# Kernel optimization log

Hardware: AMD Instinct MI355X
Metric: run time of the kernel (lower is better)

## Reference

```python
import jax, jax.numpy as jnp
import numpy as np

DROPOUT_P = 0.1


def setup_inputs() -> dict:
    key = jax.random.key(0)
    kq, kk, kv, km = jax.random.split(key, 4)
    B, H, S, D = 8, 16, 1024, 64
    query = jax.random.normal(kq, (B, H, S, D), dtype=jnp.float32)
    key_t = jax.random.normal(kk, (B, H, S, D), dtype=jnp.float32)
    value = jax.random.normal(kv, (B, H, S, D), dtype=jnp.float32)
    mask = jax.random.randint(km, (B, 1, S, S), 0, 2, dtype=jnp.int32)
    return {"query": query, "key": key_t, "value": value, "mask": mask}


def reference(query, key, value, mask):
    d_k = query.shape[-1]
    # scores: [B, H, S, S]
    scores = jnp.einsum("bhqd,bhkd->bhqk", query, key) / jnp.sqrt(
        jnp.asarray(d_k, dtype=query.dtype)
    )
    scores = jnp.where(mask == 0, jnp.asarray(-jnp.inf, dtype=scores.dtype), scores)
    attn_weights = jax.nn.softmax(scores, axis=-1)
    # deterministic dropout (train-mode semantics, fixed RNG)
    drop_key = jax.random.fold_in(jax.random.key(42), 7)
    keep = jax.random.bernoulli(drop_key, 1.0 - DROPOUT_P, attn_weights.shape)
    attn_weights = jnp.where(keep, attn_weights / (1.0 - DROPOUT_P), 0.0)
    output = jnp.einsum("bhqk,bhkd->bhqd", attn_weights, value)
    return (output, attn_weights)
```

## Files before the change

kernel.cpp:

```cpp
#include <hip/hip_runtime.h>


constexpr int Bc = 8, Hc = 16, Sc = 1024, Dc = 64;
constexpr int TQ  = 8;
constexpr int WTP = 12;

typedef float v4f __attribute__((ext_vector_type(4)));

#define TF_ROUND(x0, x1, r) { x0 += x1; x1 = ((x1 << (r)) | (x1 >> (32 - (r)))); x1 ^= x0; }

__host__ __device__ __forceinline__ void threefry2x32(unsigned k0, unsigned k1,
                                                      unsigned x0, unsigned x1,
                                                      unsigned& o0, unsigned& o1) {
  const unsigned k2 = k0 ^ k1 ^ 0x1BD11BDAu;
  x0 += k0; x1 += k1;
  TF_ROUND(x0, x1, 13) TF_ROUND(x0, x1, 15) TF_ROUND(x0, x1, 26) TF_ROUND(x0, x1, 6)
  x0 += k1; x1 += k2 + 1u;
  TF_ROUND(x0, x1, 17) TF_ROUND(x0, x1, 29) TF_ROUND(x0, x1, 16) TF_ROUND(x0, x1, 24)
  x0 += k2; x1 += k0 + 2u;
  TF_ROUND(x0, x1, 13) TF_ROUND(x0, x1, 15) TF_ROUND(x0, x1, 26) TF_ROUND(x0, x1, 6)
  x0 += k0; x1 += k1 + 3u;
  TF_ROUND(x0, x1, 17) TF_ROUND(x0, x1, 29) TF_ROUND(x0, x1, 16) TF_ROUND(x0, x1, 24)
  x0 += k1; x1 += k2 + 4u;
  TF_ROUND(x0, x1, 13) TF_ROUND(x0, x1, 15) TF_ROUND(x0, x1, 26) TF_ROUND(x0, x1, 6)
  x0 += k2; x1 += k0 + 5u;
  o0 = x0; o1 = x1;
}

__global__ __launch_bounds__(256, 4)
void attn_fused(const float* __restrict__ Qg, const float* __restrict__ Kg,
                const float* __restrict__ Vg, const int* __restrict__ Mg,
                float* __restrict__ Og, float* __restrict__ Ag,
                unsigned key0, unsigned key1)
{
  __shared__ __align__(16) float WTh[512][WTP];
  __shared__ float REDm[4][8];
  __shared__ float REDs[4][8];

  const unsigned orig = blockIdx.x;
  const unsigned wg   = (orig & 7u) * 2048u + (orig >> 3);
  const int q0 = (int)(wg & 127u) * TQ;
  const int h  = (int)(wg >> 7) & 15;
  const int b  = (int)(wg >> 11);

  const int tid = threadIdx.x;
  const int w   = tid >> 6;
  const int l   = tid & 63;
  const int kl  = w * 64 + l;
  const size_t bh = (size_t)b * Hc + h;

  const float* __restrict__ Kb = Kg + bh * Sc * Dc;
  const float* __restrict__ Vb = Vg + bh * Sc * Dc;
  const float* __restrict__ Qb = Qg + bh * Sc * Dc + (size_t)q0 * Dc;

  unsigned mbits = 0u;
  {
    const int* __restrict__ mc = Mg + (size_t)b * Sc * Sc + (size_t)q0 * Sc + kl;
    #pragma unroll
    for (int kb = 0; kb < 4; ++kb)
      #pragma unroll
      for (int q = 0; q < 8; ++q)
        mbits |= (mc[(size_t)q * Sc + kb * 256] != 0) ? (1u << (kb * 8 + q)) : 0u;
  }

  unsigned keep = 0u;
  const unsigned ibase = ((unsigned)((b * Hc + h) * Sc + q0)) * (unsigned)Sc
                         + (unsigned)kl;
  #pragma unroll 8
  for (int t2 = 0; t2 < 32; ++t2) {
    const int kb = t2 >> 3, q = t2 & 7;
    unsigned o0, o1;
    threefry2x32(key0, key1, 0u, ibase + (unsigned)(q * Sc + kb * 256), o0, o1);
    const unsigned bits = o0 ^ o1;
    const float u = __uint_as_float((bits >> 9) | 0x3f800000u) - 1.0f;
    keep |= (u < 0.9f) ? (1u << t2) : 0u;
  }

  float sv[4][8];
  #pragma unroll
  for (int kb = 0; kb < 4; ++kb)
    #pragma unroll
    for (int q = 0; q < 8; ++q) sv[kb][q] = 0.f;

  #pragma unroll 1
  for (int ds = 0; ds < 16; ++ds) {
    float4 qv[8];
    #pragma unroll
    for (int q = 0; q < 8; ++q)
      qv[q] = *(const float4*)(Qb + (size_t)q * Dc + ds * 4);
    #pragma unroll
    for (int kb = 0; kb < 4; ++kb) {
      const float4 kv = *(const float4*)(Kb + (size_t)(kb * 256 + kl) * Dc + ds * 4);
      #pragma unroll
      for (int q = 0; q < 8; ++q) {
        sv[kb][q] = fmaf(kv.x, qv[q].x, sv[kb][q]);
        sv[kb][q] = fmaf(kv.y, qv[q].y, sv[kb][q]);
        sv[kb][q] = fmaf(kv.z, qv[q].z, sv[kb][q]);
        sv[kb][q] = fmaf(kv.w, qv[q].w, sv[kb][q]);
      }
    }
  }

  const float NEG = -__builtin_inff();
  #pragma unroll
  for (int kb = 0; kb < 4; ++kb)
    #pragma unroll
    for (int q = 0; q < 8; ++q) {
      const float s = sv[kb][q] * 0.125f;
      sv[kb][q] = ((mbits >> (kb * 8 + q)) & 1u) ? s : NEG;
    }

  float mx[8];
  #pragma unroll
  for (int q = 0; q < 8; ++q) {
    float m = fmaxf(fmaxf(sv[0][q], sv[1][q]), fmaxf(sv[2][q], sv[3][q]));
    #pragma unroll
    for (int off = 32; off > 0; off >>= 1) m = fmaxf(m, __shfl_xor(m, off));
    if (l == 0) REDm[w][q] = m;
  }
  __syncthreads();
  #pragma unroll
  for (int q = 0; q < 8; ++q)
    mx[q] = fmaxf(fmaxf(REDm[0][q], REDm[1][q]), fmaxf(REDm[2][q], REDm[3][q]));

  #pragma unroll
  for (int kb = 0; kb < 4; ++kb)
    #pragma unroll
    for (int q = 0; q < 8; ++q)
      sv[kb][q] = __expf(sv[kb][q] - mx[q]);
  #pragma unroll
  for (int q = 0; q < 8; ++q) {
    float s = (sv[0][q] + sv[1][q]) + (sv[2][q] + sv[3][q]);
    #pragma unroll
    for (int off = 32; off > 0; off >>= 1) s += __shfl_xor(s, off);
    if (l == 0) REDs[w][q] = s;
  }
  __syncthreads();
  float inv9[8];
  #pragma unroll
  for (int q = 0; q < 8; ++q)
    inv9[q] = 1.0f / (((REDs[0][q] + REDs[1][q]) + (REDs[2][q] + REDs[3][q])) * 0.9f);

  float* __restrict__ Arow = Ag + bh * (size_t)Sc * Sc + (size_t)q0 * Sc + kl;
  #pragma unroll
  for (int kb = 0; kb < 4; ++kb)
    #pragma unroll
    for (int q = 0; q < 8; ++q) {
      const float wv = ((keep >> (kb * 8 + q)) & 1u) ? sv[kb][q] * inv9[q] : 0.f;
      sv[kb][q] = wv;
      __builtin_nontemporal_store(wv, &Arow[(size_t)q * Sc + kb * 256]);
    }

  const int ks = tid & 15;
  const int dq = tid >> 4;
  float4 acc[8];
  #pragma unroll
  for (int q = 0; q < 8; ++q) acc[q] = make_float4(0.f, 0.f, 0.f, 0.f);

#define ACCQ(qi, wq) { acc[qi].x = fmaf(wq, vv.x, acc[qi].x); \
                       acc[qi].y = fmaf(wq, vv.y, acc[qi].y); \
                       acc[qi].z = fmaf(wq, vv.z, acc[qi].z); \
                       acc[qi].w = fmaf(wq, vv.w, acc[qi].w); }
#define PV_COMPUTE(halfc)                                                    \
    _Pragma("unroll 4")                                                      \
    for (int i = 0; i < 32; ++i) {                                           \
      const int kr = i * 16 + ks;                                            \
      const float4 vv = *(const float4*)(Vb + (size_t)((halfc) * 512 + kr) * Dc + dq * 4); \
      const float4 lo = *(const float4*)&WTh[kr][0];                         \
      const float4 hi = *(const float4*)&WTh[kr][4];                         \
      ACCQ(0, lo.x) ACCQ(1, lo.y) ACCQ(2, lo.z) ACCQ(3, lo.w)                \
      ACCQ(4, hi.x) ACCQ(5, hi.y) ACCQ(6, hi.z) ACCQ(7, hi.w)                \
    }

  *(float4*)&WTh[kl][0]       = make_float4(sv[0][0], sv[0][1], sv[0][2], sv[0][3]);
  *(float4*)&WTh[kl][4]       = make_float4(sv[0][4], sv[0][5], sv[0][6], sv[0][7]);
  *(float4*)&WTh[256 + kl][0] = make_float4(sv[1][0], sv[1][1], sv[1][2], sv[1][3]);
  *(float4*)&WTh[256 + kl][4] = make_float4(sv[1][4], sv[1][5], sv[1][6], sv[1][7]);
  __syncthreads();
  PV_COMPUTE(0)

  __syncthreads();
  *(float4*)&WTh[kl][0]       = make_float4(sv[2][0], sv[2][1], sv[2][2], sv[2][3]);
  *(float4*)&WTh[kl][4]       = make_float4(sv[2][4], sv[2][5], sv[2][6], sv[2][7]);
  *(float4*)&WTh[256 + kl][0] = make_float4(sv[3][0], sv[3][1], sv[3][2], sv[3][3]);
  *(float4*)&WTh[256 + kl][4] = make_float4(sv[3][4], sv[3][5], sv[3][6], sv[3][7]);
  __syncthreads();
  PV_COMPUTE(1)

#undef PV_COMPUTE
#undef ACCQ

  #pragma unroll
  for (int off = 1; off <= 8; off <<= 1) {
    #pragma unroll
    for (int q = 0; q < 8; ++q) {
      acc[q].x += __shfl_xor(acc[q].x, off);
      acc[q].y += __shfl_xor(acc[q].y, off);
      acc[q].z += __shfl_xor(acc[q].z, off);
      acc[q].w += __shfl_xor(acc[q].w, off);
    }
  }
  if ((l & 15) == 0) {
    float* __restrict__ Obase = Og + bh * (size_t)Sc * Dc + (size_t)q0 * Dc + dq * 4;
    #pragma unroll
    for (int q = 0; q < 8; ++q) {
      const v4f t = { acc[q].x, acc[q].y, acc[q].z, acc[q].w };
      __builtin_nontemporal_store(t, (v4f*)(Obase + (size_t)q * Dc));
    }
  }
}

extern "C" void kernel_launch(void* const* d_in, const int* in_sizes, int n_in,
                              void* d_out, int out_size, void* d_ws, size_t ws_size,
                              hipStream_t stream) {
  const float* Qg = (const float*)d_in[0];
  const float* Kg = (const float*)d_in[1];
  const float* Vg = (const float*)d_in[2];
  const int*   Mg = (const int*)d_in[3];
  float* Og = (float*)d_out;
  float* Ag = Og + (size_t)Bc * Hc * Sc * Dc;

  unsigned k0, k1;
  threefry2x32(0u, 42u, 0u, 7u, k0, k1);

  attn_fused<<<dim3(16384), 256, 0, stream>>>(Qg, Kg, Vg, Mg, Og, Ag, k0, k1);
}
```

Baseline: 1.884 ms.

## Restructure QK dot product per key block and remap workgroups head-fastest

The QK^T loop is now done one 256-key block at a time. Each thread loads its full 64-float K row into registers and loops over the 8 query rows, with scheduling barriers separating the blocks. Previously the loop ran over 16 d-slices and kept all 32 accumulators live. The workgroup index mapping also changes so that head varies fastest instead of the query tile. This changes which blocks run concurrently and so changes how K/V and mask data are reused in cache across workgroups. Holding a 64-register K row raises register pressure, and the new mapping means consecutive blocks touch different heads' K/V while sharing mask rows.

```diff
diff --git a/kernel.cpp b/kernel.cpp
--- a/kernel.cpp
+++ b/kernel.cpp
@@ -27,6 +27,30 @@
   o0 = x0; o1 = x1;
 }
 
+template<int KB>
+__device__ __forceinline__ void qk_block(const float* __restrict__ Kb,
+                                         const float* __restrict__ Qb,
+                                         int kl, float (&svk)[8]) {
+  const float4* __restrict__ Krow = (const float4*)(Kb + (size_t)(KB * 256 + kl) * Dc);
+  float4 kr[16];
+  #pragma unroll
+  for (int j = 0; j < 16; ++j) kr[j] = Krow[j];
+  #pragma unroll
+  for (int q = 0; q < 8; ++q) {
+    const float4* __restrict__ Qrow = (const float4*)(Qb + (size_t)q * Dc);
+    float a = 0.f;
+    #pragma unroll
+    for (int j = 0; j < 16; ++j) {
+      const float4 qv = Qrow[j];
+      a = fmaf(kr[j].x, qv.x, a);
+      a = fmaf(kr[j].y, qv.y, a);
+      a = fmaf(kr[j].z, qv.z, a);
+      a = fmaf(kr[j].w, qv.w, a);
+    }
+    svk[q] = a;
+  }
+}
+
 __global__ __launch_bounds__(256, 4)
 void attn_fused(const float* __restrict__ Qg, const float* __restrict__ Kg,
                 const float* __restrict__ Vg, const int* __restrict__ Mg,
@@ -39,8 +63,8 @@
 
   const unsigned orig = blockIdx.x;
   const unsigned wg   = (orig & 7u) * 2048u + (orig >> 3);
-  const int q0 = (int)(wg & 127u) * TQ;
-  const int h  = (int)(wg >> 7) & 15;
+  const int h  = (int)(wg & 15u);
+  const int q0 = (int)((wg >> 4) & 127u) * TQ;
   const int b  = (int)(wg >> 11);
 
   const int tid = threadIdx.x;
@@ -77,29 +101,13 @@
   }
 
   float sv[4][8];
-  #pragma unroll
-  for (int kb = 0; kb < 4; ++kb)
-    #pragma unroll
-    for (int q = 0; q < 8; ++q) sv[kb][q] = 0.f;
-
-  #pragma unroll 1
-  for (int ds = 0; ds < 16; ++ds) {
-    float4 qv[8];
-    #pragma unroll
-    for (int q = 0; q < 8; ++q)
-      qv[q] = *(const float4*)(Qb + (size_t)q * Dc + ds * 4);
-    #pragma unroll
-    for (int kb = 0; kb < 4; ++kb) {
-      const float4 kv = *(const float4*)(Kb + (size_t)(kb * 256 + kl) * Dc + ds * 4);
-      #pragma unroll
-      for (int q = 0; q < 8; ++q) {
-        sv[kb][q] = fmaf(kv.x, qv[q].x, sv[kb][q]);
-        sv[kb][q] = fmaf(kv.y, qv[q].y, sv[kb][q]);
-        sv[kb][q] = fmaf(kv.z, qv[q].z, sv[kb][q]);
-        sv[kb][q] = fmaf(kv.w, qv[q].w, sv[kb][q]);
-      }
-    }
-  }
+  qk_block<0>(Kb, Qb, kl, sv[0]);
+  __builtin_amdgcn_sched_barrier(0);
+  qk_block<1>(Kb, Qb, kl, sv[1]);
+  __builtin_amdgcn_sched_barrier(0);
+  qk_block<2>(Kb, Qb, kl, sv[2]);
+  __builtin_amdgcn_sched_barrier(0);
+  qk_block<3>(Kb, Qb, kl, sv[3]);
 
   const float NEG = -__builtin_inff();
   #pragma unroll
```

Measured after the change: 4.881 ms. 159% more time.
